# Optimization experiments

Hardware: AMD Instinct MI355X
Metric: run time of the kernel (lower is better)

## Reference

```python
import jax, jax.numpy as jnp
import numpy as np

B, N, L, M, F = 32, 32, 512, 64, 64
EPS = 1e-8

def setup_inputs() -> dict:
    key = jax.random.key(0)
    k1, k2, k3, k4, k5 = jax.random.split(key, 5)
    x_aug = jax.random.normal(k1, (B, N, L, F), dtype=jnp.float32)
    # monotone time grid in [0,1], shape (L,1) so it broadcasts against (1,N,1,M)
    t = jnp.linspace(0.0, 1.0, L, dtype=jnp.float32)[:, None]
    t_left = jax.random.uniform(k2, (N, M), dtype=jnp.float32) * 0.8
    t_right = t_left + 0.05 + 0.15 * jax.random.uniform(k3, (N, M), dtype=jnp.float32)
    kappa = jax.random.normal(k4, (N, 1), dtype=jnp.float32)
    return {"x_aug": x_aug, "t": t, "t_left": t_left, "t_right": t_right, "kappa": kappa}

def reference(x_aug, t, t_left, t_right, kappa):
    # kappa: (N,1) -> softplus -> (1,N,1,1)
    k = jax.nn.softplus(kappa)[None, :, None]          # (1,N,1,1)
    tl = t_left[None, :, None, :]                       # (1,N,1,M)
    tr = t_right[None, :, None, :]                      # (1,N,1,M)
    # soft box kernel over time: alpha (1,N,L,M)
    alpha = jax.nn.sigmoid((tr - t) / k) * jax.nn.sigmoid((t - tl) / k)
    # weighted pool over L without materializing (B,N,L,M,F)
    numerator = jnp.einsum('bnlf,nlm->bnmf', x_aug, alpha[0])  # (B,N,M,F)
    denominator = alpha.sum(axis=2)[..., None]                 # (1,N,M,1)
    return numerator / (denominator + EPS)
```

## Files before the change

### kernel.cpp

```cpp
#include <hip/hip_runtime.h>
#include <math.h>

typedef unsigned short u16;
typedef unsigned int   u32;
typedef __attribute__((ext_vector_type(8))) short short8;
typedef __attribute__((ext_vector_type(4))) float f32x4;

namespace {
constexpr int Bb = 32, Nn = 32, Ll = 512, Mm = 64, Ff = 64;
constexpr int TL  = 32;
constexpr int NT  = Ll / TL;
constexpr int TLP = 40;
constexpr float EPSV = 1e-8f;
}

__device__ __forceinline__ u16 bf16rne(float x) {
    u32 u = __float_as_uint(x);
    return (u16)((u + 0x7fffu + ((u >> 16) & 1u)) >> 16);
}
__device__ __forceinline__ float bf16tof(u16 h) {
    return __uint_as_float(((u32)h) << 16);
}

__global__ __launch_bounds__(256, 4)
void wagg_fused(const float* __restrict__ x_aug,
                const float* __restrict__ t_in,
                const float* __restrict__ t_left,
                const float* __restrict__ t_right,
                const float* __restrict__ kappa,
                float* __restrict__ out)
{
    const int n   = blockIdx.x & 31;
    const int b   = blockIdx.x >> 5;
    const int tid = threadIdx.x;

    __shared__ u16 ah_s[2][Mm * TLP];
    __shared__ u16 al_s[2][Mm * TLP];
    __shared__ u16 xh_s[2][Ff * TLP];
    __shared__ u16 xl_s[2][Ff * TLP];

    const int fq  = tid & 15;
    const int lp2 = tid >> 4;

    const int wv   = tid >> 6;
    const int lane = tid & 63;
    const int ma   = wv * 16 + (lane >> 2);
    const int lqa  = lane & 3;

    const int mh = wv & 1;
    const int fh = wv >> 1;
    const int q  = lane >> 4;
    const int c  = lane & 15;

    const float* xb = x_aug + (size_t)(b * Nn + n) * (Ll * Ff);

    const float kap = kappa[n];
    const float kk  = fmaxf(kap, 0.0f) + log1pf(expf(-fabsf(kap)));
    const float ik  = 1.0f / kk;
    const float tlv = t_left [n * Mm + ma];
    const float trv = t_right[n * Mm + ma];
    const float Ac  = __expf(-trv * ik);
    const float Bc  = __expf( tlv * ik);

    f32x4 acc[2][2];
    #pragma unroll
    for (int mi = 0; mi < 2; ++mi)
        #pragma unroll
        for (int fi = 0; fi < 2; ++fi)
            acc[mi][fi] = (f32x4){0.f, 0.f, 0.f, 0.f};

    float X0[4], X1[4];
    float T[8];
    float dsum = 0.0f;

    auto stage = [&](int buf) {
        #pragma unroll
        for (int j = 0; j < 4; ++j) {
            const float v0 = X0[j], v1 = X1[j];
            const u16 h0 = bf16rne(v0), h1 = bf16rne(v1);
            const u16 s0 = bf16rne(v0 - bf16tof(h0)), s1 = bf16rne(v1 - bf16tof(h1));
            const u32 off = (u32)(fq * 4 + j) * TLP + 2 * lp2;
            *(u32*)&xh_s[buf][off] = (u32)h0 | ((u32)h1 << 16);
            *(u32*)&xl_s[buf][off] = (u32)s0 | ((u32)s1 << 16);
        }
        u32 hi[4], lo[4];
        #pragma unroll
        for (int jj = 0; jj < 8; jj += 2) {
            const float u0 = __expf(T[jj]     * ik);
            const float u1 = __expf(T[jj + 1] * ik);
            const float d0 = fmaf(Ac, u0, 1.0f) * (u0 + Bc);
            const float d1 = fmaf(Ac, u1, 1.0f) * (u1 + Bc);
            const float a0 = u0 * __builtin_amdgcn_rcpf(d0);
            const float a1 = u1 * __builtin_amdgcn_rcpf(d1);
            dsum += a0 + a1;
            const u16 h0 = bf16rne(a0), h1 = bf16rne(a1);
            const u16 s0 = bf16rne(a0 - bf16tof(h0)), s1 = bf16rne(a1 - bf16tof(h1));
            hi[jj >> 1] = (u32)h0 | ((u32)h1 << 16);
            lo[jj >> 1] = (u32)s0 | ((u32)s1 << 16);
        }
        const u32 aoff = (u32)ma * TLP + lqa * 8;
        *(uint4*)&ah_s[buf][aoff] = make_uint4(hi[0], hi[1], hi[2], hi[3]);
        *(uint4*)&al_s[buf][aoff] = make_uint4(lo[0], lo[1], lo[2], lo[3]);
    };

    {
        const float* p = xb + (size_t)(2 * lp2) * Ff + fq * 4;
        *(float4*)X0 = *(const float4*)p;
        *(float4*)X1 = *(const float4*)(p + Ff);
        *(float4*)&T[0] = *(const float4*)&t_in[lqa * 8];
        *(float4*)&T[4] = *(const float4*)&t_in[lqa * 8 + 4];
        stage(0);
    }
    __syncthreads();

    for (int tile = 0; tile < NT; ++tile) {
        const int cur = tile & 1, nxt = cur ^ 1;

        if (tile + 1 < NT) {
            const int l0 = (tile + 1) * TL;
            const float* p = xb + (size_t)(l0 + 2 * lp2) * Ff + fq * 4;
            *(float4*)X0 = *(const float4*)p;
            *(float4*)X1 = *(const float4*)(p + Ff);
            *(float4*)&T[0] = *(const float4*)&t_in[l0 + lqa * 8];
            *(float4*)&T[4] = *(const float4*)&t_in[l0 + lqa * 8 + 4];
        }

        short8 ahf[2], alf[2], xhf[2], xlf[2];
        #pragma unroll
        for (int mi = 0; mi < 2; ++mi) {
            const u32 off = (u32)(mh * 32 + mi * 16 + c) * TLP + q * 8;
            ahf[mi] = *(const short8*)&ah_s[cur][off];
            alf[mi] = *(const short8*)&al_s[cur][off];
        }
        #pragma unroll
        for (int fi = 0; fi < 2; ++fi) {
            const u32 off = (u32)(fh * 32 + fi * 16 + c) * TLP + q * 8;
            xhf[fi] = *(const short8*)&xh_s[cur][off];
            xlf[fi] = *(const short8*)&xl_s[cur][off];
        }
        #pragma unroll
        for (int mi = 0; mi < 2; ++mi)
            #pragma unroll
            for (int fi = 0; fi < 2; ++fi) {
                acc[mi][fi] = __builtin_amdgcn_mfma_f32_16x16x32_bf16(
                    ahf[mi], xhf[fi], acc[mi][fi], 0, 0, 0);
                acc[mi][fi] = __builtin_amdgcn_mfma_f32_16x16x32_bf16(
                    ahf[mi], xlf[fi], acc[mi][fi], 0, 0, 0);
                acc[mi][fi] = __builtin_amdgcn_mfma_f32_16x16x32_bf16(
                    alf[mi], xhf[fi], acc[mi][fi], 0, 0, 0);
            }

        if (tile + 1 < NT) stage(nxt);
        __syncthreads();
    }

    float* dred = (float*)&xh_s[0][0];
    float* invp = dred + 256;
    dred[lqa * 64 + ma] = dsum;
    __syncthreads();
    if (tid < Mm) {
        const float d = dred[tid] + dred[64 + tid] + dred[128 + tid] + dred[192 + tid];
        invp[tid] = __builtin_amdgcn_rcpf(d + EPSV);
    }
    __syncthreads();

    float* ob = out + (size_t)(b * Nn + n) * (Mm * Ff);
    #pragma unroll
    for (int mi = 0; mi < 2; ++mi) {
        const int mbase = mh * 32 + mi * 16 + q * 4;
        float iv[4];
        #pragma unroll
        for (int r = 0; r < 4; ++r) iv[r] = invp[mbase + r];
        #pragma unroll
        for (int fi = 0; fi < 2; ++fi) {
            const int f = fh * 32 + fi * 16 + c;
            #pragma unroll
            for (int r = 0; r < 4; ++r)
                ob[(size_t)(mbase + r) * Ff + f] = acc[mi][fi][r] * iv[r];
        }
    }
}

extern "C" void kernel_launch(void* const* d_in, const int* in_sizes, int n_in,
                              void* d_out, int out_size, void* d_ws, size_t ws_size,
                              hipStream_t stream)
{
    const float* x_aug   = (const float*)d_in[0];
    const float* t_in    = (const float*)d_in[1];
    const float* t_left  = (const float*)d_in[2];
    const float* t_right = (const float*)d_in[3];
    const float* kappa   = (const float*)d_in[4];
    float* out = (float*)d_out;

    hipLaunchKernelGGL(wagg_fused, dim3(Bb * Nn), dim3(256), 0, stream,
                       x_aug, t_in, t_left, t_right, kappa, out);
}
```

Before: 206.3 us.

## Process two batches per block to share alpha weights and deepen prefetch

```diff
diff --git a/kernel.cpp b/kernel.cpp
--- a/kernel.cpp
+++ b/kernel.cpp
@@ -22,7 +22,7 @@
     return __uint_as_float(((u32)h) << 16);
 }
 
-__global__ __launch_bounds__(256, 4)
+__global__ __launch_bounds__(256, 2)
 void wagg_fused(const float* __restrict__ x_aug,
                 const float* __restrict__ t_in,
                 const float* __restrict__ t_left,
@@ -31,152 +31,150 @@
                 float* __restrict__ out)
 {
     const int n   = blockIdx.x & 31;
-    const int b   = blockIdx.x >> 5;
+    const int b0  = (blockIdx.x >> 5) * 2;
     const int tid = threadIdx.x;
 
     __shared__ u16 ah_s[2][Mm * TLP];
     __shared__ u16 al_s[2][Mm * TLP];
-    __shared__ u16 xh_s[2][Ff * TLP];
-    __shared__ u16 xl_s[2][Ff * TLP];
+    __shared__ u16 xh_s[2][2 * Ff * TLP];
+    __shared__ u16 xl_s[2][2 * Ff * TLP];
 
     const int fq  = tid & 15;
     const int lp2 = tid >> 4;
+    const int am  = tid & 63;
+    const int aq  = tid >> 6;
 
-    const int wv   = tid >> 6;
     const int lane = tid & 63;
-    const int ma   = wv * 16 + (lane >> 2);
-    const int lqa  = lane & 3;
+    const int w    = tid >> 6;
+    const int bw   = w & 1;
+    const int mg   = w >> 1;
+    const int q    = lane >> 4;
+    const int c    = lane & 15;
 
-    const int mh = wv & 1;
-    const int fh = wv >> 1;
-    const int q  = lane >> 4;
-    const int c  = lane & 15;
-
-    const float* xb = x_aug + (size_t)(b * Nn + n) * (Ll * Ff);
+    const float* xb0 = x_aug + (size_t)(b0 * Nn + n) * (Ll * Ff);
+    const float* xb1 = x_aug + (size_t)((b0 + 1) * Nn + n) * (Ll * Ff);
 
     const float kap = kappa[n];
     const float kk  = fmaxf(kap, 0.0f) + log1pf(expf(-fabsf(kap)));
     const float ik  = 1.0f / kk;
-    const float tlv = t_left [n * Mm + ma];
-    const float trv = t_right[n * Mm + ma];
+    const float tlv = t_left [n * Mm + am];
+    const float trv = t_right[n * Mm + am];
     const float Ac  = __expf(-trv * ik);
     const float Bc  = __expf( tlv * ik);
 
-    f32x4 acc[2][2];
+    f32x4 acc[2][4];
     #pragma unroll
     for (int mi = 0; mi < 2; ++mi)
         #pragma unroll
-        for (int fi = 0; fi < 2; ++fi)
-            acc[mi][fi] = (f32x4){0.f, 0.f, 0.f, 0.f};
+        for (int ft = 0; ft < 4; ++ft)
+            acc[mi][ft] = (f32x4){0.f, 0.f, 0.f, 0.f};
 
-    float X0[4], X1[4];
-    float T[8];
+    float Xr[2][2][2][4];
+    float Tr[2][8];
     float dsum = 0.0f;
 
-    auto stage = [&](int buf) {
+    auto load_tile = [&](int tile, int rb) {
+        const size_t row = (size_t)(tile * TL + 2 * lp2) * Ff + fq * 4;
+        *(float4*)Xr[rb][0][0] = *(const float4*)(xb0 + row);
+        *(float4*)Xr[rb][0][1] = *(const float4*)(xb0 + row + Ff);
+        *(float4*)Xr[rb][1][0] = *(const float4*)(xb1 + row);
+        *(float4*)Xr[rb][1][1] = *(const float4*)(xb1 + row + Ff);
+        *(float4*)&Tr[rb][0] = *(const float4*)&t_in[tile * TL + aq * 8];
+        *(float4*)&Tr[rb][4] = *(const float4*)&t_in[tile * TL + aq * 8 + 4];
+    };
+
+    auto stage_tile = [&](int rb, int sb) {
         #pragma unroll
-        for (int j = 0; j < 4; ++j) {
-            const float v0 = X0[j], v1 = X1[j];
-            const u16 h0 = bf16rne(v0), h1 = bf16rne(v1);
-            const u16 s0 = bf16rne(v0 - bf16tof(h0)), s1 = bf16rne(v1 - bf16tof(h1));
-            const u32 off = (u32)(fq * 4 + j) * TLP + 2 * lp2;
-            *(u32*)&xh_s[buf][off] = (u32)h0 | ((u32)h1 << 16);
-            *(u32*)&xl_s[buf][off] = (u32)s0 | ((u32)s1 << 16);
-        }
+        for (int bi = 0; bi < 2; ++bi)
+            #pragma unroll
+            for (int j = 0; j < 4; ++j) {
+                const float v0 = Xr[rb][bi][0][j], v1 = Xr[rb][bi][1][j];
+                const u16 h0 = bf16rne(v0), h1 = bf16rne(v1);
+                const u16 s0 = bf16rne(v0 - bf16tof(h0)), s1 = bf16rne(v1 - bf16tof(h1));
+                const u32 off = (u32)(bi * Ff + fq * 4 + j) * TLP + 2 * lp2;
+                *(u32*)&xh_s[sb][off] = (u32)h0 | ((u32)h1 << 16);
+                *(u32*)&xl_s[sb][off] = (u32)s0 | ((u32)s1 << 16);
+            }
         u32 hi[4], lo[4];
         #pragma unroll
         for (int jj = 0; jj < 8; jj += 2) {
-            const float u0 = __expf(T[jj]     * ik);
-            const float u1 = __expf(T[jj + 1] * ik);
-            const float d0 = fmaf(Ac, u0, 1.0f) * (u0 + Bc);
-            const float d1 = fmaf(Ac, u1, 1.0f) * (u1 + Bc);
-            const float a0 = u0 * __builtin_amdgcn_rcpf(d0);
-            const float a1 = u1 * __builtin_amdgcn_rcpf(d1);
+            const float u0 = __expf(Tr[rb][jj]     * ik);
+            const float u1 = __expf(Tr[rb][jj + 1] * ik);
+            const float a0 = u0 * __builtin_amdgcn_rcpf(fmaf(Ac, u0, 1.0f) * (u0 + Bc));
+            const float a1 = u1 * __builtin_amdgcn_rcpf(fmaf(Ac, u1, 1.0f) * (u1 + Bc));
             dsum += a0 + a1;
             const u16 h0 = bf16rne(a0), h1 = bf16rne(a1);
             const u16 s0 = bf16rne(a0 - bf16tof(h0)), s1 = bf16rne(a1 - bf16tof(h1));
             hi[jj >> 1] = (u32)h0 | ((u32)h1 << 16);
             lo[jj >> 1] = (u32)s0 | ((u32)s1 << 16);
         }
-        const u32 aoff = (u32)ma * TLP + lqa * 8;
-        *(uint4*)&ah_s[buf][aoff] = make_uint4(hi[0], hi[1], hi[2], hi[3]);
-        *(uint4*)&al_s[buf][aoff] = make_uint4(lo[0], lo[1], lo[2], lo[3]);
+        const u32 aoff = (u32)am * TLP + aq * 8;
+        *(uint4*)&ah_s[sb][aoff] = make_uint4(hi[0], hi[1], hi[2], hi[3]);
+        *(uint4*)&al_s[sb][aoff] = make_uint4(lo[0], lo[1], lo[2], lo[3]);
     };
 
-    {
-        const float* p = xb + (size_t)(2 * lp2) * Ff + fq * 4;
-        *(float4*)X0 = *(const float4*)p;
-        *(float4*)X1 = *(const float4*)(p + Ff);
-        *(float4*)&T[0] = *(const float4*)&t_in[lqa * 8];
-        *(float4*)&T[4] = *(const float4*)&t_in[lqa * 8 + 4];
-        stage(0);
-    }
+    load_tile(0, 0);
+    stage_tile(0, 0);
+    load_tile(1, 0);
     __syncthreads();
 
-    for (int tile = 0; tile < NT; ++tile) {
-        const int cur = tile & 1, nxt = cur ^ 1;
+    for (int t = 0; t < NT; ++t) {
+        const int cur = t & 1, nxt = cur ^ 1;
 
-        if (tile + 1 < NT) {
-            const int l0 = (tile + 1) * TL;
-            const float* p = xb + (size_t)(l0 + 2 * lp2) * Ff + fq * 4;
-            *(float4*)X0 = *(const float4*)p;
-            *(float4*)X1 = *(const float4*)(p + Ff);
-            *(float4*)&T[0] = *(const float4*)&t_in[l0 + lqa * 8];
-            *(float4*)&T[4] = *(const float4*)&t_in[l0 + lqa * 8 + 4];
-        }
+        if (t + 2 < NT) load_tile(t + 2, nxt);
 
-        short8 ahf[2], alf[2], xhf[2], xlf[2];
+        short8 ahf[2], alf[2], xhf[4], xlf[4];
         #pragma unroll
         for (int mi = 0; mi < 2; ++mi) {
-            const u32 off = (u32)(mh * 32 + mi * 16 + c) * TLP + q * 8;
+            const u32 off = (u32)((mg * 2 + mi) * 16 + c) * TLP + q * 8;
             ahf[mi] = *(const short8*)&ah_s[cur][off];
             alf[mi] = *(const short8*)&al_s[cur][off];
         }
         #pragma unroll
-        for (int fi = 0; fi < 2; ++fi) {
-            const u32 off = (u32)(fh * 32 + fi * 16 + c) * TLP + q * 8;
-            xhf[fi] = *(const short8*)&xh_s[cur][off];
-            xlf[fi] = *(const short8*)&xl_s[cur][off];
+        for (int ft = 0; ft < 4; ++ft) {
+            const u32 off = (u32)(bw * Ff + ft * 16 + c) * TLP + q * 8;
+            xhf[ft] = *(const short8*)&xh_s[cur][off];
+            xlf[ft] = *(const short8*)&xl_s[cur][off];
         }
         #pragma unroll
         for (int mi = 0; mi < 2; ++mi)
             #pragma unroll
-            for (int fi = 0; fi < 2; ++fi) {
-                acc[mi][fi] = __builtin_amdgcn_mfma_f32_16x16x32_bf16(
-                    ahf[mi], xhf[fi], acc[mi][fi], 0, 0, 0);
-                acc[mi][fi] = __builtin_amdgcn_mfma_f32_16x16x32_bf16(
-                    ahf[mi], xlf[fi], acc[mi][fi], 0, 0, 0);
-                acc[mi][fi] = __builtin_amdgcn_mfma_f32_16x16x32_bf16(
-                    alf[mi], xhf[fi], acc[mi][fi], 0, 0, 0);
+            for (int ft = 0; ft < 4; ++ft) {
+                acc[mi][ft] = __builtin_amdgcn_mfma_f32_16x16x32_bf16(
+                    ahf[mi], xhf[ft], acc[mi][ft], 0, 0, 0);
+                acc[mi][ft] = __builtin_amdgcn_mfma_f32_16x16x32_bf16(
+                    ahf[mi], xlf[ft], acc[mi][ft], 0, 0, 0);
+                acc[mi][ft] = __builtin_amdgcn_mfma_f32_16x16x32_bf16(
+                    alf[mi], xhf[ft], acc[mi][ft], 0, 0, 0);
             }
 
-        if (tile + 1 < NT) stage(nxt);
+        if (t + 1 < NT) stage_tile(cur, nxt);
         __syncthreads();
     }
 
     float* dred = (float*)&xh_s[0][0];
     float* invp = dred + 256;
-    dred[lqa * 64 + ma] = dsum;
+    dred[aq * 64 + am] = dsum;
     __syncthreads();
     if (tid < Mm) {
         const float d = dred[tid] + dred[64 + tid] + dred[128 + tid] + dred[192 + tid];
-        invp[tid] = __builtin_amdgcn_rcpf(d + EPSV);
+        invp[tid] = 1.0f / (d + EPSV);
     }
     __syncthreads();
 
-    float* ob = out + (size_t)(b * Nn + n) * (Mm * Ff);
+    float* ob = out + (size_t)((b0 + bw) * Nn + n) * (Mm * Ff);
     #pragma unroll
     for (int mi = 0; mi < 2; ++mi) {
-        const int mbase = mh * 32 + mi * 16 + q * 4;
+        const int mbase = (mg * 2 + mi) * 16 + q * 4;
         float iv[4];
         #pragma unroll
         for (int r = 0; r < 4; ++r) iv[r] = invp[mbase + r];
         #pragma unroll
-        for (int fi = 0; fi < 2; ++fi) {
-            const int f = fh * 32 + fi * 16 + c;
+        for (int ft = 0; ft < 4; ++ft) {
+            const int f = ft * 16 + c;
             #pragma unroll
             for (int r = 0; r < 4; ++r)
-                ob[(size_t)(mbase + r) * Ff + f] = acc[mi][fi][r] * iv[r];
+                ob[(size_t)(mbase + r) * Ff + f] = acc[mi][ft][r] * iv[r];
         }
     }
 }
@@ -192,6 +190,6 @@
     const float* kappa   = (const float*)d_in[4];
     float* out = (float*)d_out;
 
-    hipLaunchKernelGGL(wagg_fused, dim3(Bb * Nn), dim3(256), 0, stream,
+    hipLaunchKernelGGL(wagg_fused, dim3((Bb / 2) * Nn), dim3(256), 0, stream,
                        x_aug, t_in, t_left, t_right, kappa, out);
 }
```

After: 230.5 us. 1.12x slower.
